# Performance work log

Hardware: AMD Instinct MI355X
Metric: run time of the kernel (lower is better)

## Reference

```python
import jax, jax.numpy as jnp
import numpy as np

B, T, D = 4, 4096, 64

def setup_inputs() -> dict:
    key = jax.random.key(0)
    k1, k2, k3 = jax.random.split(key, 3)
    x = jax.random.normal(k1, (B, T, D), dtype=jnp.float32)
    # att_dense1 kernel (zeros init in source; use small random for a meaningful baseline)
    W1 = jax.random.normal(k2, (D, D), dtype=jnp.float32) * 0.05
    b1 = jnp.zeros((D,), dtype=jnp.float32)
    # att_dense2 kernel: glorot_normal
    W2 = jax.random.normal(k3, (D, D), dtype=jnp.float32) * jnp.sqrt(2.0 / (D + D))
    b2 = jnp.zeros((D,), dtype=jnp.float32)
    return {"x": x, "W1": W1, "b1": b1, "W2": W2, "b2": b2}

def reference(x, W1, b1, W2, b2):
    # Per-timestep MLP: Dense(D, softmax) -> Dense(D, tanh)
    h1 = jax.nn.softmax(jnp.einsum('btd,de->bte', x, W1) + b1, axis=-1)
    encoded = jnp.tanh(jnp.einsum('btd,de->bte', h1, W2) + b2)  # [B,T,D]
    # scores[b,i,j] = <x[b,i], encoded[b,j]>
    scores = jnp.einsum('bid,bjd->bij', x, encoded)             # [B,T,T]
    attention = jax.nn.softmax(scores, axis=-1)
    # K.permute_dimensions(attention,(0,2,1)) then batch_dot with x:
    # out[b,i,d] = sum_j attention[b,j,i] * x[b,j,d]
    return jnp.einsum('bji,bjd->bid', attention, x)             # [B,T,D]
```

## Files before the change

### kernel.cpp

```cpp
#include <hip/hip_runtime.h>


typedef _Float16 f16;
typedef __attribute__((ext_vector_type(8))) _Float16 f16x8;
typedef __attribute__((ext_vector_type(4))) _Float16 f16x4;
typedef __attribute__((ext_vector_type(4))) float f32x4;

#define TT 4096
#define BB 4
#define BT (BB*TT)
#define SPLIT_A 16

#define MFMA32(A,B,C) __builtin_amdgcn_mfma_f32_16x16x32_f16(A,B,C,0,0,0)
#define MFMA16(A,B,C) __builtin_amdgcn_mfma_f32_16x16x16f16(A,B,C,0,0,0)

#if __has_builtin(__builtin_amdgcn_exp2f)
#define EXP2F(x) __builtin_amdgcn_exp2f(x)
#else
#define EXP2F(x) exp2f(x)
#endif

#define LOG2E 1.4426950408889634f

__global__ __launch_bounds__(256) void k_wpack(
    const float* __restrict__ W1, const float* __restrict__ W2,
    f16* __restrict__ w1fh, f16* __restrict__ w1fl,
    f16* __restrict__ w2fh, f16* __restrict__ w2fl) {
  int tid = threadIdx.x;
#pragma unroll
  for (int k2 = 0; k2 < 2; ++k2) {
    int idx = tid * 2 + k2;
    int l15 = idx & 15, quad = (idx >> 4) & 3, kc = (idx >> 6) & 1, mtW = idx >> 7;
    f16 h8[8], l8[8];
#pragma unroll
    for (int t = 0; t < 8; ++t) {
      float v = W1[(size_t)(kc * 32 + quad * 8 + t) * 64 + mtW * 16 + l15];
      f16 h = (f16)v;
      h8[t] = h; l8[t] = (f16)(v - (float)h);
    }
    *(f16x8*)(w1fh + (size_t)idx * 8) = *(f16x8*)h8;
    *(f16x8*)(w1fl + (size_t)idx * 8) = *(f16x8*)l8;
  }
#pragma unroll
  for (int k4 = 0; k4 < 4; ++k4) {
    int idx = tid * 4 + k4;
    int l15 = idx & 15, quad = (idx >> 4) & 3, kt = (idx >> 6) & 3, mt2 = idx >> 8;
    f16 h4[4], l4[4];
#pragma unroll
    for (int t = 0; t < 4; ++t) {
      float v = W2[(size_t)(kt * 16 + quad * 4 + t) * 64 + mt2 * 16 + l15];
      f16 h = (f16)v;
      h4[t] = h; l4[t] = (f16)(v - (float)h);
    }
    *(f16x4*)(w2fh + (size_t)idx * 4) = *(f16x4*)h4;
    *(f16x4*)(w2fl + (size_t)idx * 4) = *(f16x4*)l4;
  }
}

__global__ __launch_bounds__(256, 1) void k_encode(
    const float* __restrict__ x,
    const float* __restrict__ b1, const float* __restrict__ b2,
    const f16* __restrict__ w1fh, const f16* __restrict__ w1fl,
    const f16* __restrict__ w2fh, const f16* __restrict__ w2fl,
    f16* __restrict__ ench, f16* __restrict__ encl,
    f16* __restrict__ xafh, f16* __restrict__ xafl, f16* __restrict__ xtf,
    float* __restrict__ Zbuf) {
  __shared__ float xS[4][16][68];
  __shared__ float encS[4][16][68];
  int tid = threadIdx.x;
  int w = tid >> 6, lane = tid & 63, quad = lane >> 4, l15 = lane & 15;
  if (tid < 64) Zbuf[blockIdx.x * 64 + tid] = 0.f;
  int slice = blockIdx.x * 4 + w;
  int base = slice * 16;
  f16x8 w1h[4][2], w1l[4][2];
#pragma unroll
  for (int mt = 0; mt < 4; ++mt)
#pragma unroll
    for (int kc = 0; kc < 2; ++kc) {
      size_t off = (size_t)(((mt * 2 + kc) * 4 + quad) * 16 + l15) * 8;
      w1h[mt][kc] = *(const f16x8*)(w1fh + off);
      w1l[mt][kc] = *(const f16x8*)(w1fl + off);
    }
  f16x4 w2h[4][4], w2l[4][4];
#pragma unroll
  for (int mt = 0; mt < 4; ++mt)
#pragma unroll
    for (int kt = 0; kt < 4; ++kt) {
      size_t off = (size_t)(((mt * 4 + kt) * 4 + quad) * 16 + l15) * 4;
      w2h[mt][kt] = *(const f16x4*)(w2fh + off);
      w2l[mt][kt] = *(const f16x4*)(w2fl + off);
    }
  f16x8 xbh[2], xbl[2];
#pragma unroll
  for (int kc = 0; kc < 2; ++kc) {
    const float4* p = (const float4*)(x + (size_t)(base + l15) * 64 + kc * 32 + quad * 8);
    float4 v0 = p[0], v1 = p[1];
    float v[8] = {v0.x, v0.y, v0.z, v0.w, v1.x, v1.y, v1.z, v1.w};
    f16 h8[8], l8[8];
#pragma unroll
    for (int t = 0; t < 8; ++t) {
      f16 h = (f16)v[t];
      h8[t] = h; l8[t] = (f16)(v[t] - (float)h);
    }
    xbh[kc] = *(f16x8*)h8;
    xbl[kc] = *(f16x8*)l8;
    size_t off = (size_t)slice * 1024 + kc * 512 + quad * 128 + l15 * 8;
    *(f16x8*)(xafh + off) = xbh[kc];
    *(f16x8*)(xafl + off) = xbl[kc];
    *(float4*)&xS[w][l15][kc * 32 + quad * 8] = v0;
    *(float4*)&xS[w][l15][kc * 32 + quad * 8 + 4] = v1;
  }
  f32x4 acc1[4];
#pragma unroll
  for (int mt = 0; mt < 4; ++mt) {
    f32x4 z = {0.f, 0.f, 0.f, 0.f};
    acc1[mt] = z;
  }
#pragma unroll
  for (int kc = 0; kc < 2; ++kc)
#pragma unroll
    for (int mt = 0; mt < 4; ++mt) {
      acc1[mt] = MFMA32(w1h[mt][kc], xbh[kc], acc1[mt]);
      acc1[mt] = MFMA32(w1h[mt][kc], xbl[kc], acc1[mt]);
      acc1[mt] = MFMA32(w1l[mt][kc], xbh[kc], acc1[mt]);
    }
  float h1[4][4];
#pragma unroll
  for (int mt = 0; mt < 4; ++mt) {
    float4 bv = *(const float4*)(b1 + mt * 16 + quad * 4);
    h1[mt][0] = acc1[mt][0] + bv.x;
    h1[mt][1] = acc1[mt][1] + bv.y;
    h1[mt][2] = acc1[mt][2] + bv.z;
    h1[mt][3] = acc1[mt][3] + bv.w;
  }
  float m1 = h1[0][0];
#pragma unroll
  for (int mt = 0; mt < 4; ++mt)
#pragma unroll
    for (int r = 0; r < 4; ++r) m1 = fmaxf(m1, h1[mt][r]);
  m1 = fmaxf(m1, __shfl_xor(m1, 16));
  m1 = fmaxf(m1, __shfl_xor(m1, 32));
  float ssum = 0.f;
  float ev[4][4];
#pragma unroll
  for (int mt = 0; mt < 4; ++mt)
#pragma unroll
    for (int r = 0; r < 4; ++r) {
      ev[mt][r] = EXP2F((h1[mt][r] - m1) * LOG2E);
      ssum += ev[mt][r];
    }
  ssum += __shfl_xor(ssum, 16);
  ssum += __shfl_xor(ssum, 32);
  float rs = __builtin_amdgcn_rcpf(ssum);
  f16x4 p1h[4], p1l[4];
#pragma unroll
  for (int mt = 0; mt < 4; ++mt)
#pragma unroll
    for (int r = 0; r < 4; ++r) {
      float p = ev[mt][r] * rs;
      f16 h = (f16)p;
      p1h[mt][r] = h;
      p1l[mt][r] = (f16)(p - (float)h);
    }
  f32x4 acc2[4];
#pragma unroll
  for (int mt = 0; mt < 4; ++mt) {
    f32x4 z = {0.f, 0.f, 0.f, 0.f};
    acc2[mt] = z;
  }
#pragma unroll
  for (int kt = 0; kt < 4; ++kt)
#pragma unroll
    for (int mt = 0; mt < 4; ++mt) {
      acc2[mt] = MFMA16(w2h[mt][kt], p1h[kt], acc2[mt]);
      acc2[mt] = MFMA16(w2h[mt][kt], p1l[kt], acc2[mt]);
      acc2[mt] = MFMA16(w2l[mt][kt], p1h[kt], acc2[mt]);
    }
#pragma unroll
  for (int mt = 0; mt < 4; ++mt) {
    float4 bv = *(const float4*)(b2 + mt * 16 + quad * 4);
    float bb[4] = {bv.x, bv.y, bv.z, bv.w};
    float o4[4];
#pragma unroll
    for (int r = 0; r < 4; ++r) {
      float hv = acc2[mt][r] + bb[r];
      float ex = EXP2F(hv * (2.0f * LOG2E));
      float th = 1.0f - 2.0f * __builtin_amdgcn_rcpf(ex + 1.0f);
      o4[r] = th * LOG2E;
    }
    *(float4*)&encS[w][l15][mt * 16 + quad * 4] = *(float4*)o4;
  }
#pragma unroll
  for (int k = 0; k < 2; ++k) {
    int e = k * 64 + lane;
    int n = e & 15, quad2 = (e >> 4) & 3, kc = e >> 6;
    const float4* p = (const float4*)&encS[w][n][kc * 32 + quad2 * 8];
    float4 v0 = p[0], v1 = p[1];
    float v[8] = {v0.x, v0.y, v0.z, v0.w, v1.x, v1.y, v1.z, v1.w};
    f16 h8[8], l8[8];
#pragma unroll
    for (int t = 0; t < 8; ++t) {
      f16 h = (f16)v[t];
      h8[t] = h; l8[t] = (f16)(v[t] - (float)h);
    }
    *(f16x8*)(ench + ((size_t)slice * 128 + e) * 8) = *(f16x8*)h8;
    *(f16x8*)(encl + ((size_t)slice * 128 + e) * 8) = *(f16x8*)l8;
  }
  int b = slice >> 8, ls = slice & 255;
#pragma unroll
  for (int k = 0; k < 4; ++k) {
    f16 p8[8];
#pragma unroll
    for (int t = 0; t < 4; ++t) {
      float v = xS[w][k * 4 + t][lane];
      f16 h = (f16)v;
      p8[t] = h; p8[4 + t] = (f16)(v - (float)h);
    }
    size_t off = ((((size_t)b * (TT / 16) + ls) * 4 + k) * 64 + lane) * 8;
    *(f16x8*)(xtf + off) = *(f16x8*)p8;
  }
}

__global__ __launch_bounds__(512, 4) void k_statsM(
    const f16* __restrict__ xafh, const f16* __restrict__ ench,
    float* __restrict__ Zbuf) {
  int tid = threadIdx.x;
  int w = tid >> 6, lane = tid & 63, quad = lane >> 4, l15 = lane & 15;
  int jb = blockIdx.x * 256 + w * 32;
  int b = jb >> 12;
  f16x8 xa[2][2];
#pragma unroll
  for (int mt = 0; mt < 2; ++mt)
#pragma unroll
    for (int kc = 0; kc < 2; ++kc) {
      size_t off = (size_t)((jb >> 4) + mt) * 1024 + kc * 512 + quad * 128 + l15 * 8;
      xa[mt][kc] = *(const f16x8*)(xafh + off);
    }
  float l_run[8];
#pragma unroll
  for (int s = 0; s < 8; ++s) l_run[s] = 0.f;
  int i0 = blockIdx.y * (TT / SPLIT_A);
  size_t ebase = (size_t)((b * TT + i0) >> 4) * 1024 + quad * 128 + l15 * 8;
  const f16* pEh = ench + ebase;
  for (int it = 0; it < TT / SPLIT_A / 64; ++it) {
    f32x4 acc[2][4];
#pragma unroll
    for (int mt = 0; mt < 2; ++mt)
#pragma unroll
      for (int nt = 0; nt < 4; ++nt) {
        f32x4 z = {0.f, 0.f, 0.f, 0.f};
        acc[mt][nt] = z;
      }
#pragma unroll
    for (int kc = 0; kc < 2; ++kc) {
      f16x8 ebf[4];
#pragma unroll
      for (int nt = 0; nt < 4; ++nt)
        ebf[nt] = *(const f16x8*)(pEh + nt * 1024 + kc * 512);
#pragma unroll
      for (int mt = 0; mt < 2; ++mt)
#pragma unroll
        for (int nt = 0; nt < 4; ++nt)
          acc[mt][nt] = MFMA32(xa[mt][kc], ebf[nt], acc[mt][nt]);
    }
#pragma unroll
    for (int mt = 0; mt < 2; ++mt)
#pragma unroll
      for (int r = 0; r < 4; ++r)
        l_run[mt * 4 + r] += EXP2F(acc[mt][0][r]) + EXP2F(acc[mt][1][r]) +
                             EXP2F(acc[mt][2][r]) + EXP2F(acc[mt][3][r]);
    pEh += 4096;
  }
#pragma unroll
  for (int s = 0; s < 8; ++s) {
    float l = l_run[s];
#pragma unroll
    for (int off = 1; off < 16; off <<= 1) l += __shfl_xor(l, off);
    l_run[s] = l;
  }
  if (l15 == 0) {
#pragma unroll
    for (int mt = 0; mt < 2; ++mt)
#pragma unroll
      for (int r = 0; r < 4; ++r)
        atomicAdd(Zbuf + jb + mt * 16 + quad * 4 + r, l_run[mt * 4 + r]);
  }
}

__global__ __launch_bounds__(512, 4) void k_outB(
    const f16* __restrict__ xafh, const f16* __restrict__ xafl,
    const f16* __restrict__ xtf,
    const f16* __restrict__ ench, const f16* __restrict__ encl,
    const float* __restrict__ Zv, float* __restrict__ slabs, int jlen) {
  int tid = threadIdx.x;
  int w = tid >> 6, lane = tid & 63, quad = lane >> 4, l15 = lane & 15;
  int ibase = blockIdx.x * 256;
  int iw = ibase + w * 32;
  int b = ibase >> 12;
  f16x8 ebr[2][2][2];
#pragma unroll
  for (int nt = 0; nt < 2; ++nt)
#pragma unroll
    for (int kc = 0; kc < 2; ++kc) {
      size_t off = (size_t)((iw >> 4) + nt) * 1024 + kc * 512 + quad * 128 + l15 * 8;
      ebr[nt][kc][0] = *(const f16x8*)(ench + off);
      ebr[nt][kc][1] = *(const f16x8*)(encl + off);
    }
  f32x4 oacc[2][4];
#pragma unroll
  for (int nt = 0; nt < 2; ++nt)
#pragma unroll
    for (int mtb = 0; mtb < 4; ++mtb) {
      f32x4 z = {0.f, 0.f, 0.f, 0.f};
      oacc[nt][mtb] = z;
    }
  int jt0 = blockIdx.y * jlen;
  int nit = jlen / 16;
  size_t jf0 = (size_t)b * TT + jt0;
  const f16* pAh = xafh + (jf0 >> 4) * 1024 + quad * 128 + l15 * 8;
  const f16* pAl = xafl + (jf0 >> 4) * 1024 + quad * 128 + l15 * 8;
  const f16* pPV = xtf + ((size_t)b * (TT / 16) + (jt0 >> 4)) * 2048 +
                   quad * 512 + l15 * 8;
  const float* pZ = Zv + jf0 + quad * 4;
  f16x8 cah[2], cal[2];
  cah[0] = *(const f16x8*)(pAh);       cah[1] = *(const f16x8*)(pAh + 512);
  cal[0] = *(const f16x8*)(pAl);       cal[1] = *(const f16x8*)(pAl + 512);
  pAh += 1024; pAl += 1024;
  for (int t = 0; t < nit; ++t) {
    f16x8 pv[4];
#pragma unroll
    for (int mtb = 0; mtb < 4; ++mtb)
      pv[mtb] = *(const f16x8*)(pPV + mtb * 128);
    float rz[4];
#pragma unroll
    for (int r = 0; r < 4; ++r)
      rz[r] = __builtin_amdgcn_rcpf(pZ[r]);
    f16x8 nah[2], nal[2];
    nah[0] = *(const f16x8*)(pAh);     nah[1] = *(const f16x8*)(pAh + 512);
    nal[0] = *(const f16x8*)(pAl);     nal[1] = *(const f16x8*)(pAl + 512);
    f32x4 sacc[2];
#pragma unroll
    for (int nt = 0; nt < 2; ++nt) {
      f32x4 z = {0.f, 0.f, 0.f, 0.f};
      sacc[nt] = z;
    }
#pragma unroll
    for (int kc = 0; kc < 2; ++kc)
#pragma unroll
      for (int nt = 0; nt < 2; ++nt) {
        sacc[nt] = MFMA32(cah[kc], ebr[nt][kc][0], sacc[nt]);
        sacc[nt] = MFMA32(cah[kc], ebr[nt][kc][1], sacc[nt]);
        sacc[nt] = MFMA32(cal[kc], ebr[nt][kc][0], sacc[nt]);
      }
    f16x4 pbh[2];
#pragma unroll
    for (int nt = 0; nt < 2; ++nt)
#pragma unroll
      for (int r = 0; r < 4; ++r)
        pbh[nt][r] = (f16)(EXP2F(sacc[nt][r]) * rz[r]);
#pragma unroll
    for (int mtb = 0; mtb < 4; ++mtb) {
      f16x4 bh = {pv[mtb][0], pv[mtb][1], pv[mtb][2], pv[mtb][3]};
      f16x4 bl = {pv[mtb][4], pv[mtb][5], pv[mtb][6], pv[mtb][7]};
#pragma unroll
      for (int nt = 0; nt < 2; ++nt) {
        oacc[nt][mtb] = MFMA16(pbh[nt], bh, oacc[nt][mtb]);
        oacc[nt][mtb] = MFMA16(pbh[nt], bl, oacc[nt][mtb]);
      }
    }
    cah[0] = nah[0]; cah[1] = nah[1];
    cal[0] = nal[0]; cal[1] = nal[1];
    pAh += 1024; pAl += 1024; pPV += 2048; pZ += 16;
  }
  float* slab = slabs + (size_t)blockIdx.y * BT * 64;
#pragma unroll
  for (int nt = 0; nt < 2; ++nt)
#pragma unroll
    for (int r = 0; r < 4; ++r) {
      int i = iw + nt * 16 + quad * 4 + r;
#pragma unroll
      for (int mtb = 0; mtb < 4; ++mtb)
        slab[(size_t)i * 64 + mtb * 16 + l15] = oacc[nt][mtb][r];
    }
}

__global__ __launch_bounds__(256) void k_reduce(const float* __restrict__ slabs,
                                                float* __restrict__ out,
                                                int nsplit) {
  int e = (blockIdx.x * 256 + threadIdx.x) * 4;
  float4 acc = *(const float4*)(slabs + e);
  for (int s = 1; s < nsplit; ++s) {
    float4 v = *(const float4*)(slabs + (size_t)s * BT * 64 + e);
    acc.x += v.x; acc.y += v.y; acc.z += v.z; acc.w += v.w;
  }
  *(float4*)(out + e) = acc;
}

extern "C" void kernel_launch(void* const* d_in, const int* in_sizes, int n_in,
                              void* d_out, int out_size, void* d_ws,
                              size_t ws_size, hipStream_t stream) {
  const float* x = (const float*)d_in[0];
  const float* W1 = (const float*)d_in[1];
  const float* b1 = (const float*)d_in[2];
  const float* W2 = (const float*)d_in[3];
  const float* b2 = (const float*)d_in[4];
  float* out = (float*)d_out;

  f16* xafh = (f16*)d_ws;
  f16* xafl = xafh + (size_t)BT * 64;
  f16* xtf  = xafl + (size_t)BT * 64;
  f16* ench = xtf + (size_t)BT * 128;
  f16* encl = ench + (size_t)BT * 64;
  float* Zv = (float*)(encl + (size_t)BT * 64);
  f16* w1fh = (f16*)(Zv + BT);
  f16* w1fl = w1fh + 4096;
  f16* w2fh = w1fl + 4096;
  f16* w2fl = w2fh + 4096;
  float* slabs = (float*)(w2fl + 4096);

  size_t base_bytes = (size_t)((char*)slabs - (char*)d_ws);
  size_t slab_bytes = (size_t)BT * 64 * sizeof(float);
  int nsplit = 8;
  while (nsplit > 1 && base_bytes + (size_t)nsplit * slab_bytes > ws_size)
    nsplit >>= 1;

  k_wpack<<<dim3(1), dim3(256), 0, stream>>>(W1, W2, w1fh, w1fl, w2fh, w2fl);
  k_encode<<<dim3(BT / 64), dim3(256), 0, stream>>>(
      x, b1, b2, w1fh, w1fl, w2fh, w2fl, ench, encl, xafh, xafl, xtf, Zv);
  k_statsM<<<dim3(BT / 256, SPLIT_A), dim3(512), 0, stream>>>(xafh, ench, Zv);
  k_outB<<<dim3(BT / 256, nsplit), dim3(512), 0, stream>>>(
      xafh, xafl, xtf, ench, encl, Zv, slabs, TT / nsplit);
  k_reduce<<<dim3(BT * 64 / 1024), dim3(256), 0, stream>>>(slabs, out, nsplit);
}
```

Measured before the change: 140.5 us.

## Software-pipeline score MFMAs one tile ahead of PV accumulation in k_outB

Restructures the k_outB inner loop so the score MFMAs for the next j-tile are issued while the exp/normalise and PV MFMAs of the current tile run. A prologue computes the first score tile. The loop is unrolled by two with ping-pong register buffers for the A operand, loaded two tiles ahead, and the Z value is carried one tile ahead. The aim is to hide the dependency between the score MFMAs and the exp chain, and to hide global-load latency. In exchange it keeps more registers live under a tight launch bound, assumes an even iteration count, and reads A and Z past the end of the j range.

```diff
diff --git a/kernel.cpp b/kernel.cpp
--- a/kernel.cpp
+++ b/kernel.cpp
@@ -287,6 +287,46 @@
   }
 }
 
+#define OUTB_SUBITER(STH, STL, SOH, SOL)                                     \
+  {                                                                          \
+    f16x8 pvc[4];                                                            \
+    _Pragma("unroll") for (int mtb = 0; mtb < 4; ++mtb)                      \
+        pvc[mtb] = *(const f16x8*)(pPV + mtb * 128);                         \
+    float nz[4];                                                             \
+    _Pragma("unroll") for (int r = 0; r < 4; ++r) nz[r] = pZ[r];             \
+    SOH[0] = *(const f16x8*)(pAh);                                           \
+    SOH[1] = *(const f16x8*)(pAh + 512);                                     \
+    SOL[0] = *(const f16x8*)(pAl);                                           \
+    SOL[1] = *(const f16x8*)(pAl + 512);                                     \
+    pAh += 1024; pAl += 1024; pPV += 2048; pZ += 16;                         \
+    float rz[4];                                                             \
+    _Pragma("unroll") for (int r = 0; r < 4; ++r)                            \
+        rz[r] = __builtin_amdgcn_rcpf(zc[r]);                                \
+    f16x4 pbh[2];                                                            \
+    _Pragma("unroll") for (int nt = 0; nt < 2; ++nt)                         \
+      _Pragma("unroll") for (int r = 0; r < 4; ++r)                          \
+          pbh[nt][r] = (f16)(EXP2F(sacc[nt][r]) * rz[r]);                    \
+    _Pragma("unroll") for (int nt = 0; nt < 2; ++nt) {                       \
+      f32x4 zz = {0.f, 0.f, 0.f, 0.f};                                      \
+      sacc[nt] = zz;                                                         \
+    }                                                                        \
+    _Pragma("unroll") for (int kc = 0; kc < 2; ++kc)                         \
+      _Pragma("unroll") for (int nt = 0; nt < 2; ++nt) {                     \
+        sacc[nt] = MFMA32(STH[kc], ebr[nt][kc][0], sacc[nt]);                \
+        sacc[nt] = MFMA32(STH[kc], ebr[nt][kc][1], sacc[nt]);                \
+        sacc[nt] = MFMA32(STL[kc], ebr[nt][kc][0], sacc[nt]);                \
+      }                                                                      \
+    _Pragma("unroll") for (int mtb = 0; mtb < 4; ++mtb) {                    \
+      f16x4 bh = {pvc[mtb][0], pvc[mtb][1], pvc[mtb][2], pvc[mtb][3]};       \
+      f16x4 bl = {pvc[mtb][4], pvc[mtb][5], pvc[mtb][6], pvc[mtb][7]};       \
+      _Pragma("unroll") for (int nt = 0; nt < 2; ++nt) {                     \
+        oacc[nt][mtb] = MFMA16(pbh[nt], bh, oacc[nt][mtb]);                  \
+        oacc[nt][mtb] = MFMA16(pbh[nt], bl, oacc[nt][mtb]);                  \
+      }                                                                      \
+    }                                                                        \
+    _Pragma("unroll") for (int r = 0; r < 4; ++r) zc[r] = nz[r];             \
+  }
+
 __global__ __launch_bounds__(512, 4) void k_outB(
     const f16* __restrict__ xafh, const f16* __restrict__ xafl,
     const f16* __restrict__ xtf,
@@ -322,55 +362,32 @@
   const f16* pPV = xtf + ((size_t)b * (TT / 16) + (jt0 >> 4)) * 2048 +
                    quad * 512 + l15 * 8;
   const float* pZ = Zv + jf0 + quad * 4;
-  f16x8 cah[2], cal[2];
-  cah[0] = *(const f16x8*)(pAh);       cah[1] = *(const f16x8*)(pAh + 512);
-  cal[0] = *(const f16x8*)(pAl);       cal[1] = *(const f16x8*)(pAl + 512);
-  pAh += 1024; pAl += 1024;
-  for (int t = 0; t < nit; ++t) {
-    f16x8 pv[4];
-#pragma unroll
-    for (int mtb = 0; mtb < 4; ++mtb)
-      pv[mtb] = *(const f16x8*)(pPV + mtb * 128);
-    float rz[4];
-#pragma unroll
-    for (int r = 0; r < 4; ++r)
-      rz[r] = __builtin_amdgcn_rcpf(pZ[r]);
-    f16x8 nah[2], nal[2];
-    nah[0] = *(const f16x8*)(pAh);     nah[1] = *(const f16x8*)(pAh + 512);
-    nal[0] = *(const f16x8*)(pAl);     nal[1] = *(const f16x8*)(pAl + 512);
-    f32x4 sacc[2];
+  f16x8 aAh[2], aAl[2], aBh[2], aBl[2];
+  aAh[0] = *(const f16x8*)(pAh);        aAh[1] = *(const f16x8*)(pAh + 512);
+  aAl[0] = *(const f16x8*)(pAl);        aAl[1] = *(const f16x8*)(pAl + 512);
+  aBh[0] = *(const f16x8*)(pAh + 1024); aBh[1] = *(const f16x8*)(pAh + 1536);
+  aBl[0] = *(const f16x8*)(pAl + 1024); aBl[1] = *(const f16x8*)(pAl + 1536);
+  float zc[4];
+#pragma unroll
+  for (int r = 0; r < 4; ++r) zc[r] = pZ[r];
+  pAh += 2048; pAl += 2048; pZ += 16;
+  f32x4 sacc[2];
+#pragma unroll
+  for (int nt = 0; nt < 2; ++nt) {
+    f32x4 z = {0.f, 0.f, 0.f, 0.f};
+    sacc[nt] = z;
+  }
+#pragma unroll
+  for (int kc = 0; kc < 2; ++kc)
 #pragma unroll
     for (int nt = 0; nt < 2; ++nt) {
-      f32x4 z = {0.f, 0.f, 0.f, 0.f};
-      sacc[nt] = z;
-    }
-#pragma unroll
-    for (int kc = 0; kc < 2; ++kc)
-#pragma unroll
-      for (int nt = 0; nt < 2; ++nt) {
-        sacc[nt] = MFMA32(cah[kc], ebr[nt][kc][0], sacc[nt]);
-        sacc[nt] = MFMA32(cah[kc], ebr[nt][kc][1], sacc[nt]);
-        sacc[nt] = MFMA32(cal[kc], ebr[nt][kc][0], sacc[nt]);
-      }
-    f16x4 pbh[2];
-#pragma unroll
-    for (int nt = 0; nt < 2; ++nt)
-#pragma unroll
-      for (int r = 0; r < 4; ++r)
-        pbh[nt][r] = (f16)(EXP2F(sacc[nt][r]) * rz[r]);
-#pragma unroll
-    for (int mtb = 0; mtb < 4; ++mtb) {
-      f16x4 bh = {pv[mtb][0], pv[mtb][1], pv[mtb][2], pv[mtb][3]};
-      f16x4 bl = {pv[mtb][4], pv[mtb][5], pv[mtb][6], pv[mtb][7]};
-#pragma unroll
-      for (int nt = 0; nt < 2; ++nt) {
-        oacc[nt][mtb] = MFMA16(pbh[nt], bh, oacc[nt][mtb]);
-        oacc[nt][mtb] = MFMA16(pbh[nt], bl, oacc[nt][mtb]);
-      }
-    }
-    cah[0] = nah[0]; cah[1] = nah[1];
-    cal[0] = nal[0]; cal[1] = nal[1];
-    pAh += 1024; pAl += 1024; pPV += 2048; pZ += 16;
+      sacc[nt] = MFMA32(aAh[kc], ebr[nt][kc][0], sacc[nt]);
+      sacc[nt] = MFMA32(aAh[kc], ebr[nt][kc][1], sacc[nt]);
+      sacc[nt] = MFMA32(aAl[kc], ebr[nt][kc][0], sacc[nt]);
+    }
+  for (int t = 0; t < nit; t += 2) {
+    OUTB_SUBITER(aBh, aBl, aAh, aAl)
+    OUTB_SUBITER(aAh, aAl, aBh, aBl)
   }
   float* slab = slabs + (size_t)blockIdx.y * BT * 64;
 #pragma unroll
```

Measured after the change: 167.9 us. 19.5% more time.
